# Optimization experiments

Hardware: AMD Instinct MI355X
Metric: run time of the kernel (lower is better)

The kernel has to match this reference:

```python
import jax, jax.numpy as jnp
import numpy as np

D_MODEL = 1024
N_HEADS = 16
D_K = D_MODEL // N_HEADS
THETA = 10000.0
BATCH = 2
SEQ = 2048


def apply_rope(x, positions):
    # x: [B, H, S, d_k], positions: [S] int
    half = D_K // 2
    inv_freq = 1.0 / (THETA ** (jnp.arange(half, dtype=jnp.float32) * 2.0 / D_K))  # [half]
    ang = positions.astype(jnp.float32)[:, None] * inv_freq[None, :]  # [S, half]
    cos = jnp.cos(ang)
    sin = jnp.sin(ang)
    xr = x.reshape(x.shape[:-1] + (half, 2))
    x1, x2 = xr[..., 0], xr[..., 1]
    o1 = x1 * cos - x2 * sin
    o2 = x1 * sin + x2 * cos
    return jnp.stack([o1, o2], axis=-1).reshape(x.shape)


def setup_inputs() -> dict:
    key = jax.random.key(0)
    ks = jax.random.split(key, 5)
    scale = 1.0 / np.sqrt(D_MODEL)
    return {
        "x": jax.random.normal(ks[0], (BATCH, SEQ, D_MODEL), jnp.float32),
        "token_positions": jnp.arange(SEQ, dtype=jnp.int32),
        "Wq": jax.random.normal(ks[1], (D_MODEL, D_MODEL), jnp.float32) * scale,
        "Wk": jax.random.normal(ks[2], (D_MODEL, D_MODEL), jnp.float32) * scale,
        "Wv": jax.random.normal(ks[3], (D_MODEL, D_MODEL), jnp.float32) * scale,
        "Wo": jax.random.normal(ks[4], (D_MODEL, D_MODEL), jnp.float32) * scale,
    }


def reference(x, token_positions, Wq, Wk, Wv, Wo):
    B, S, _ = x.shape
    # projections (Linear with weight [out, in], no bias): y = x @ W^T
    def split_heads(t):
        return t.reshape(B, S, N_HEADS, D_K).transpose(0, 2, 1, 3)  # [B,H,S,d_k]

    Q = split_heads(x @ Wq.T)
    K = split_heads(x @ Wk.T)
    V = split_heads(x @ Wv.T)

    Q = apply_rope(Q, token_positions)
    K = apply_rope(K, token_positions)

    scores = jnp.einsum("bhqd,bhkd->bhqk", Q, K) / np.sqrt(D_K)
    causal = jnp.tril(jnp.ones((S, S), dtype=bool))
    scores = jnp.where(causal, scores, -jnp.inf)
    attn = jax.nn.softmax(scores, axis=-1)
    out = jnp.einsum("bhqk,bhkd->bhqd", attn, V)  # [B,H,S,d_k]
    out = out.transpose(0, 2, 1, 3).reshape(B, S, D_MODEL)
    return out @ Wo.T
```

## Files before the change

kernel.cpp:

```cpp
#include <hip/hip_runtime.h>
#include <hip/hip_bf16.h>


typedef __bf16 bf16x8 __attribute__((ext_vector_type(8)));
typedef __bf16 bf16x4 __attribute__((ext_vector_type(4)));
typedef float f32x4 __attribute__((ext_vector_type(4)));
typedef unsigned short ushort8 __attribute__((ext_vector_type(8)));

#define BATCH 2
#define SEQ 2048
#define NH 16
#define DK 64
#define DM 1024
#define BH (BATCH*NH)
#define M_TOT (BATCH*SEQ)
#define QB 128

__device__ __forceinline__ void gload16(const void* g, void* l) {
    __builtin_amdgcn_global_load_lds((const __attribute__((address_space(1))) void*)g,
                                     (__attribute__((address_space(3))) void*)l, 16, 0, 0);
}

__global__ void cvt_kernel(const float* __restrict__ s, __bf16* __restrict__ d, int n) {
    int i = (blockIdx.x * blockDim.x + threadIdx.x) * 4;
    if (i >= n) return;
    float4 v = *(const float4*)(s + i);
    bf16x4 o;
    o[0] = (__bf16)v.x; o[1] = (__bf16)v.y; o[2] = (__bf16)v.z; o[3] = (__bf16)v.w;
    *(bf16x4*)(d + i) = o;
}

__global__ void cvt4_kernel(const float* __restrict__ s0, const float* __restrict__ s1,
                            const float* __restrict__ s2, const float* __restrict__ s3,
                            __bf16* __restrict__ d0, __bf16* __restrict__ d1,
                            __bf16* __restrict__ d2, __bf16* __restrict__ d3, int n) {
    const int z = blockIdx.y;
    const float* s = (z == 0) ? s0 : (z == 1) ? s1 : (z == 2) ? s2 : s3;
    __bf16* d = (z == 0) ? d0 : (z == 1) ? d1 : (z == 2) ? d2 : d3;
    int i = (blockIdx.x * blockDim.x + threadIdx.x) * 4;
    if (i >= n) return;
    float4 v = *(const float4*)(s + i);
    bf16x4 o;
    o[0] = (__bf16)v.x; o[1] = (__bf16)v.y; o[2] = (__bf16)v.z; o[3] = (__bf16)v.w;
    *(bf16x4*)(d + i) = o;
}

__device__ __forceinline__ void gemm_tile_compute(
    const __bf16* __restrict__ A, const __bf16* __restrict__ W,
    int m0, int n0, int K, __bf16* sA, __bf16* sB, f32x4 (&acc)[4][4])
{
    const int t = threadIdx.x;
    const int lane = t & 63, wid = t >> 6;
    const int wr = wid >> 1, wc = wid & 1;
    const int g = lane >> 4, l15 = lane & 15;

    f32x4 zero = {0.f, 0.f, 0.f, 0.f};
#pragma unroll
    for (int mt = 0; mt < 4; ++mt)
#pragma unroll
        for (int nt = 0; nt < 4; ++nt) acc[mt][nt] = zero;

    for (int k0 = 0; k0 < K; k0 += 32) {
        __syncthreads();
#pragma unroll
        for (int rnd = 0; rnd < 2; ++rnd) {
            int s = rnd * 256 + t;
            int row = s >> 2, ch = s & 3;
            __bf16* dstA = sA + (rnd * 256 + wid * 64) * 8;
            __bf16* dstB = sB + (rnd * 256 + wid * 64) * 8;
            gload16(A + (size_t)(m0 + row) * K + k0 + ch * 8, dstA);
            gload16(W + (size_t)(n0 + row) * K + k0 + ch * 8, dstB);
        }
        __syncthreads();
        bf16x8 af[4], bfr[4];
#pragma unroll
        for (int mt = 0; mt < 4; ++mt)
            af[mt] = *(const bf16x8*)&sA[(wr * 64 + mt * 16 + l15) * 32 + g * 8];
#pragma unroll
        for (int nt = 0; nt < 4; ++nt)
            bfr[nt] = *(const bf16x8*)&sB[(wc * 64 + nt * 16 + l15) * 32 + g * 8];
#pragma unroll
        for (int mt = 0; mt < 4; ++mt)
#pragma unroll
            for (int nt = 0; nt < 4; ++nt)
                acc[mt][nt] = __builtin_amdgcn_mfma_f32_16x16x32_bf16(af[mt], bfr[nt], acc[mt][nt], 0, 0, 0);
    }
}

__global__ __launch_bounds__(256) void gemm_qkv(
    const __bf16* __restrict__ xb,
    const __bf16* __restrict__ wq, const __bf16* __restrict__ wk, const __bf16* __restrict__ wv,
    __bf16* __restrict__ Qb, __bf16* __restrict__ Kb, __bf16* __restrict__ VTb)
{
    __shared__ __align__(16) __bf16 sA[128 * 32], sB[128 * 32];
    const int z = blockIdx.z;
    const __bf16* W = (z == 0) ? wq : ((z == 1) ? wk : wv);
    f32x4 acc[4][4];
    const int m0 = blockIdx.y * 128, n0 = blockIdx.x * 128;
    gemm_tile_compute(xb, W, m0, n0, DM, sA, sB, acc);

    const int t = threadIdx.x, lane = t & 63, wid = t >> 6;
    const int wr = wid >> 1, wc = wid & 1, g = lane >> 4, l15 = lane & 15;
    __bf16* QK = (z == 0) ? Qb : Kb;
#pragma unroll
    for (int mt = 0; mt < 4; ++mt)
#pragma unroll
        for (int nt = 0; nt < 4; ++nt)
#pragma unroll
            for (int r = 0; r < 4; ++r) {
                int m = m0 + wr * 64 + mt * 16 + g * 4 + r;
                int n = n0 + wc * 64 + nt * 16 + l15;
                int b = m >> 11, s = m & 2047, h = n >> 6, d = n & 63;
                __bf16 v = (__bf16)acc[mt][nt][r];
                if (z < 2)
                    QK[(((size_t)(b * NH + h)) * SEQ + s) * DK + d] = v;
                else
                    VTb[(((size_t)(b * NH + h)) * DK + d) * SEQ + s] = v;
            }
}

__global__ __launch_bounds__(256) void gemm_out(
    const __bf16* __restrict__ AO, const __bf16* __restrict__ wo, float* __restrict__ out)
{
    __shared__ __align__(16) __bf16 sA[128 * 32], sB[128 * 32];
    f32x4 acc[4][4];
    const int m0 = blockIdx.y * 128, n0 = blockIdx.x * 128;
    gemm_tile_compute(AO, wo, m0, n0, DM, sA, sB, acc);

    const int t = threadIdx.x, lane = t & 63, wid = t >> 6;
    const int wr = wid >> 1, wc = wid & 1, g = lane >> 4, l15 = lane & 15;
#pragma unroll
    for (int mt = 0; mt < 4; ++mt)
#pragma unroll
        for (int nt = 0; nt < 4; ++nt)
#pragma unroll
            for (int r = 0; r < 4; ++r) {
                int m = m0 + wr * 64 + mt * 16 + g * 4 + r;
                int n = n0 + wc * 64 + nt * 16 + l15;
                out[(size_t)m * DM + n] = acc[mt][nt][r];
            }
}

__global__ __launch_bounds__(256) void rope_kernel(
    __bf16* __restrict__ Qb, __bf16* __restrict__ Kb, const int* __restrict__ pos)
{
    __shared__ float ctab[32], stab[32];
    const int s = blockIdx.x;
    const int t = threadIdx.x;
    if (t < 32) {
        float invf = exp2f(-13.287712379549449f * (float)t * (1.0f / 32.0f));
        float ang = (float)pos[s] * invf;
        float sn, cs;
        sincosf(ang, &sn, &cs);
        ctab[t] = cs; stab[t] = sn;
    }
    __syncthreads();
#pragma unroll
    for (int u = 0; u < 8; ++u) {
        int id = u * 256 + t;
        int i = id & 31;
        int bh = (id >> 5) & 31;
        __bf16* P = (id >> 10) ? Kb : Qb;
        __bf16* p = P + ((size_t)bh * SEQ + s) * DK + i * 2;
        float x1 = (float)p[0], x2 = (float)p[1];
        float c = ctab[i], sn = stab[i];
        p[0] = (__bf16)(x1 * c - x2 * sn);
        p[1] = (__bf16)(x1 * sn + x2 * c);
    }
}

__global__ __launch_bounds__(256, 3) void attn_kernel(
    const __bf16* __restrict__ Qb, const __bf16* __restrict__ Kb,
    const __bf16* __restrict__ VTb, __bf16* __restrict__ AO)
{
    __shared__ __align__(16) __bf16 sK[2][64 * 64];
    __shared__ __align__(16) __bf16 sV[2][64 * 64];
    __shared__ __align__(16) __bf16 sP[4 * 2 * 16 * 64];

    const int n = blockIdx.x + 16 * blockIdx.y;
    const int xcd = n & 7, slot = n >> 3;
    const int bh = xcd * 4 + (slot >> 4);
    const int j = 15 - (slot & 15);
    const int t = threadIdx.x, lane = t & 63, wid = t >> 6;
    const int g = lane >> 4, l15 = lane & 15;

    const size_t baseQK = (size_t)bh * SEQ * DK;
    const size_t baseVT = (size_t)bh * DK * SEQ;
    const int b = bh >> 4, h = bh & 15;
    const int qrow_w = j * QB + wid * 32;

    bf16x8 qf[2][2];
#pragma unroll
    for (int s = 0; s < 2; ++s) {
        const __bf16* qp = Qb + baseQK + (size_t)(qrow_w + s * 16 + l15) * DK;
        qf[s][0] = *(const bf16x8*)(qp + g * 8);
        qf[s][1] = *(const bf16x8*)(qp + 32 + g * 8);
    }

    f32x4 zero = {0.f, 0.f, 0.f, 0.f};
    f32x4 oacc[2][4];
    float mrow[2][4], lrow[2][4];
#pragma unroll
    for (int s = 0; s < 2; ++s)
#pragma unroll
        for (int r = 0; r < 4; ++r) {
            oacc[s][r] = zero;
        }
#pragma unroll
    for (int s = 0; s < 2; ++s)
#pragma unroll
        for (int dt = 0; dt < 4; ++dt) oacc[s][dt] = zero;
#pragma unroll
    for (int s = 0; s < 2; ++s)
#pragma unroll
        for (int r = 0; r < 4; ++r) { mrow[s][r] = -3e38f; lrow[s][r] = 0.f; }

    const char* Kt0 = (const char*)(Kb + baseQK);
    const char* Vt0 = (const char*)(VTb + baseVT);
    const int ktmax = 2 * j + 1;

    auto stage_tile = [&](int kt, int bq) {
        const char* Kt = Kt0 + (size_t)kt * 64 * 128;
        const char* Vt = Vt0 + (size_t)kt * 128;
#pragma unroll
        for (int cc = 0; cc < 2; ++cc) {
            int c = t + cc * 256;
            int r = c >> 3, pp = c & 7;
            int p = pp ^ (r & 7);
            char* bK = (char*)sK[bq] + (cc * 256 + wid * 64) * 16;
            char* bV = (char*)sV[bq] + (cc * 256 + wid * 64) * 16;
            gload16(Kt + (size_t)r * 128 + p * 16, bK);
            gload16(Vt + (size_t)r * (SEQ * 2) + p * 16, bV);
        }
    };

    stage_tile(0, 0);
    __syncthreads();
    int cur = 0;

    for (int kt = 0; kt <= ktmax; ++kt) {
        if (kt < ktmax) stage_tile(kt + 1, cur ^ 1);

        f32x4 sacc[2][4];
#pragma unroll
        for (int s = 0; s < 2; ++s)
#pragma unroll
            for (int nt = 0; nt < 4; ++nt) sacc[s][nt] = zero;
#pragma unroll
        for (int nt = 0; nt < 4; ++nt) {
            int row = nt * 16 + l15;
#pragma unroll
            for (int ks = 0; ks < 2; ++ks) {
                bf16x8 kf = *(const bf16x8*)((const char*)sK[cur] + row * 128 +
                                             ((ks * 64 + g * 16) ^ ((row & 7) << 4)));
                sacc[0][nt] = __builtin_amdgcn_mfma_f32_16x16x32_bf16(qf[0][ks], kf, sacc[0][nt], 0, 0, 0);
                sacc[1][nt] = __builtin_amdgcn_mfma_f32_16x16x32_bf16(qf[1][ks], kf, sacc[1][nt], 0, 0, 0);
            }
        }

#pragma unroll
        for (int s = 0; s < 2; ++s) {
            const int q0 = qrow_w + s * 16;
            if (kt * 64 + 63 > q0) {
#pragma unroll
                for (int nt = 0; nt < 4; ++nt)
#pragma unroll
                    for (int r = 0; r < 4; ++r) {
                        int kv = kt * 64 + nt * 16 + l15;
                        int q = q0 + g * 4 + r;
                        if (kv > q) sacc[s][nt][r] = -3e38f; else sacc[s][nt][r] *= 0.125f;
                    }
            } else {
#pragma unroll
                for (int nt = 0; nt < 4; ++nt)
#pragma unroll
                    for (int r = 0; r < 4; ++r) sacc[s][nt][r] *= 0.125f;
            }
#pragma unroll
            for (int r = 0; r < 4; ++r) {
                float tm = fmaxf(fmaxf(sacc[s][0][r], sacc[s][1][r]),
                                 fmaxf(sacc[s][2][r], sacc[s][3][r]));
#pragma unroll
                for (int msk = 1; msk < 16; msk <<= 1) tm = fmaxf(tm, __shfl_xor(tm, msk));
                float mnew = fmaxf(mrow[s][r], tm);
                float sc = __expf(mrow[s][r] - mnew);
                float rs = 0.f;
#pragma unroll
                for (int nt = 0; nt < 4; ++nt) {
                    float p = __expf(sacc[s][nt][r] - mnew);
                    sacc[s][nt][r] = p;
                    rs += p;
                }
#pragma unroll
                for (int msk = 1; msk < 16; msk <<= 1) rs += __shfl_xor(rs, msk);
                lrow[s][r] = lrow[s][r] * sc + rs;
                mrow[s][r] = mnew;
#pragma unroll
                for (int dt = 0; dt < 4; ++dt) oacc[s][dt][r] *= sc;
            }
            char* myP = (char*)sP + (wid * 2 + s) * 2048;
#pragma unroll
            for (int nt = 0; nt < 4; ++nt)
#pragma unroll
                for (int r = 0; r < 4; ++r) {
                    int row = g * 4 + r;
                    *(__bf16*)(myP + row * 128 +
                               ((nt * 32 + l15 * 2) ^ ((row & 7) << 4))) = (__bf16)sacc[s][nt][r];
                }
        }

#pragma unroll
        for (int ks = 0; ks < 2; ++ks) {
            bf16x8 pf[2];
#pragma unroll
            for (int s = 0; s < 2; ++s)
                pf[s] = *(const bf16x8*)((char*)sP + (wid * 2 + s) * 2048 + l15 * 128 +
                                         ((ks * 64 + g * 16) ^ ((l15 & 7) << 4)));
#pragma unroll
            for (int dt = 0; dt < 4; ++dt) {
                int row = dt * 16 + l15;
                bf16x8 vf = *(const bf16x8*)((const char*)sV[cur] + row * 128 +
                                             ((ks * 64 + g * 16) ^ ((row & 7) << 4)));
                oacc[0][dt] = __builtin_amdgcn_mfma_f32_16x16x32_bf16(pf[0], vf, oacc[0][dt], 0, 0, 0);
                oacc[1][dt] = __builtin_amdgcn_mfma_f32_16x16x32_bf16(pf[1], vf, oacc[1][dt], 0, 0, 0);
            }
        }

        __syncthreads();
        cur ^= 1;
    }

#pragma unroll
    for (int s = 0; s < 2; ++s)
#pragma unroll
        for (int r = 0; r < 4; ++r) {
            float inv = 1.0f / lrow[s][r];
            int srow = qrow_w + s * 16 + g * 4 + r;
            size_t obase = ((size_t)b * SEQ + srow) * DM + h * DK;
#pragma unroll
            for (int dt = 0; dt < 4; ++dt)
                AO[obase + dt * 16 + l15] = (__bf16)(oacc[s][dt][r] * inv);
        }
}

extern "C" void kernel_launch(void* const* d_in, const int* in_sizes, int n_in,
                              void* d_out, int out_size, void* d_ws, size_t ws_size,
                              hipStream_t stream) {
    (void)in_sizes; (void)n_in; (void)out_size; (void)ws_size;
    const float* x  = (const float*)d_in[0];
    const int*  pos = (const int*)d_in[1];
    const float* Wq = (const float*)d_in[2];
    const float* Wk = (const float*)d_in[3];
    const float* Wv = (const float*)d_in[4];
    const float* Wo = (const float*)d_in[5];
    float* out = (float*)d_out;

    char* ws = (char*)d_ws;
    __bf16* xb  = (__bf16*)ws; ws += (size_t)M_TOT * DM * 2;
    __bf16* wqb = (__bf16*)ws; ws += (size_t)DM * DM * 2;
    __bf16* wkb = (__bf16*)ws; ws += (size_t)DM * DM * 2;
    __bf16* wvb = (__bf16*)ws; ws += (size_t)DM * DM * 2;
    __bf16* wob = (__bf16*)ws; ws += (size_t)DM * DM * 2;
    __bf16* Qb  = (__bf16*)ws; ws += (size_t)BH * SEQ * DK * 2;
    __bf16* Kb  = (__bf16*)ws; ws += (size_t)BH * SEQ * DK * 2;
    __bf16* VTb = (__bf16*)ws; ws += (size_t)BH * SEQ * DK * 2;
    __bf16* AOb = (__bf16*)ws; ws += (size_t)M_TOT * DM * 2;

    const int nx = M_TOT * DM, nw = DM * DM;
    cvt_kernel<<<nx / 4 / 256, 256, 0, stream>>>(x, xb, nx);
    cvt4_kernel<<<dim3(nw / 4 / 256, 4), 256, 0, stream>>>(Wq, Wk, Wv, Wo, wqb, wkb, wvb, wob, nw);

    gemm_qkv<<<dim3(DM / 128, M_TOT / 128, 3), 256, 0, stream>>>(xb, wqb, wkb, wvb, Qb, Kb, VTb);
    rope_kernel<<<SEQ, 256, 0, stream>>>(Qb, Kb, pos);
    attn_kernel<<<dim3(16, BH), 256, 0, stream>>>(Qb, Kb, VTb, AOb);
    gemm_out<<<dim3(DM / 128, M_TOT / 128), 256, 0, stream>>>(AOb, wob, out);
}
```

Measured before the change: 269.3 us.

## Widen GEMM K-tile with swizzled LDS, fuse QKV weights, pair attention query blocks

The shared GEMM tile now stages 64-wide K chunks into XOR-swizzled LDS, which halves the number of barrier rounds and avoids bank conflicts. Q/K/V weights go into one contiguous buffer, so a single 2D grid with XCD-aware block remapping covers all three projections, and gemm_out gets the same remap. The attention kernel launches 256 blocks, each handling a short and a long causal query block (j and 15-j) to balance work per block, and the occupancy hint of 3 is dropped. The wider LDS tiles and the loss of the occupancy bound may reduce waves per CU.

```diff
diff --git a/kernel.cpp b/kernel.cpp
--- a/kernel.cpp
+++ b/kernel.cpp
@@ -60,48 +60,57 @@
 #pragma unroll
         for (int nt = 0; nt < 4; ++nt) acc[mt][nt] = zero;
 
-    for (int k0 = 0; k0 < K; k0 += 32) {
+    for (int k0 = 0; k0 < K; k0 += 64) {
         __syncthreads();
 #pragma unroll
-        for (int rnd = 0; rnd < 2; ++rnd) {
-            int s = rnd * 256 + t;
-            int row = s >> 2, ch = s & 3;
-            __bf16* dstA = sA + (rnd * 256 + wid * 64) * 8;
-            __bf16* dstB = sB + (rnd * 256 + wid * 64) * 8;
-            gload16(A + (size_t)(m0 + row) * K + k0 + ch * 8, dstA);
-            gload16(W + (size_t)(n0 + row) * K + k0 + ch * 8, dstB);
+        for (int rnd = 0; rnd < 4; ++rnd) {
+            int slot = rnd * 256 + t;
+            int row = slot >> 3, pp = slot & 7;
+            int p = pp ^ (row & 7);
+            char* dA = (char*)sA + (rnd * 256 + wid * 64) * 16;
+            char* dB = (char*)sB + (rnd * 256 + wid * 64) * 16;
+            gload16((const char*)(A + (size_t)(m0 + row) * K + k0) + p * 16, dA);
+            gload16((const char*)(W + (size_t)(n0 + row) * K + k0) + p * 16, dB);
         }
         __syncthreads();
-        bf16x8 af[4], bfr[4];
-#pragma unroll
-        for (int mt = 0; mt < 4; ++mt)
-            af[mt] = *(const bf16x8*)&sA[(wr * 64 + mt * 16 + l15) * 32 + g * 8];
-#pragma unroll
-        for (int nt = 0; nt < 4; ++nt)
-            bfr[nt] = *(const bf16x8*)&sB[(wc * 64 + nt * 16 + l15) * 32 + g * 8];
-#pragma unroll
-        for (int mt = 0; mt < 4; ++mt)
-#pragma unroll
-            for (int nt = 0; nt < 4; ++nt)
-                acc[mt][nt] = __builtin_amdgcn_mfma_f32_16x16x32_bf16(af[mt], bfr[nt], acc[mt][nt], 0, 0, 0);
+#pragma unroll
+        for (int ks = 0; ks < 2; ++ks) {
+            bf16x8 af[4], bfr[4];
+#pragma unroll
+            for (int mt = 0; mt < 4; ++mt) {
+                int row = wr * 64 + mt * 16 + l15;
+                af[mt] = *(const bf16x8*)((char*)sA + row * 128 +
+                                          ((ks * 64 + g * 16) ^ ((row & 7) << 4)));
+            }
+#pragma unroll
+            for (int nt = 0; nt < 4; ++nt) {
+                int row = wc * 64 + nt * 16 + l15;
+                bfr[nt] = *(const bf16x8*)((char*)sB + row * 128 +
+                                           ((ks * 64 + g * 16) ^ ((row & 7) << 4)));
+            }
+#pragma unroll
+            for (int mt = 0; mt < 4; ++mt)
+#pragma unroll
+                for (int nt = 0; nt < 4; ++nt)
+                    acc[mt][nt] = __builtin_amdgcn_mfma_f32_16x16x32_bf16(af[mt], bfr[nt], acc[mt][nt], 0, 0, 0);
+        }
     }
 }
 
 __global__ __launch_bounds__(256) void gemm_qkv(
-    const __bf16* __restrict__ xb,
-    const __bf16* __restrict__ wq, const __bf16* __restrict__ wk, const __bf16* __restrict__ wv,
+    const __bf16* __restrict__ xb, const __bf16* __restrict__ wqkv,
     __bf16* __restrict__ Qb, __bf16* __restrict__ Kb, __bf16* __restrict__ VTb)
 {
-    __shared__ __align__(16) __bf16 sA[128 * 32], sB[128 * 32];
-    const int z = blockIdx.z;
-    const __bf16* W = (z == 0) ? wq : ((z == 1) ? wk : wv);
+    __shared__ __align__(16) __bf16 sA[128 * 64], sB[128 * 64];
+    int id = blockIdx.x + 24 * blockIdx.y;
+    id = (id & 7) * 96 + (id >> 3);
+    const int m0 = (id / 24) * 128, n0 = (id % 24) * 128;
+
     f32x4 acc[4][4];
-    const int m0 = blockIdx.y * 128, n0 = blockIdx.x * 128;
-    gemm_tile_compute(xb, W, m0, n0, DM, sA, sB, acc);
+    gemm_tile_compute(xb, wqkv, m0, n0, DM, sA, sB, acc);
 
     const int t = threadIdx.x, lane = t & 63, wid = t >> 6;
     const int wr = wid >> 1, wc = wid & 1, g = lane >> 4, l15 = lane & 15;
-    __bf16* QK = (z == 0) ? Qb : Kb;
 #pragma unroll
     for (int mt = 0; mt < 4; ++mt)
 #pragma unroll
@@ -110,10 +119,13 @@
             for (int r = 0; r < 4; ++r) {
                 int m = m0 + wr * 64 + mt * 16 + g * 4 + r;
                 int n = n0 + wc * 64 + nt * 16 + l15;
-                int b = m >> 11, s = m & 2047, h = n >> 6, d = n & 63;
+                int z = n >> 10, hd = n & 1023, h = hd >> 6, d = hd & 63;
+                int b = m >> 11, s = m & 2047;
                 __bf16 v = (__bf16)acc[mt][nt][r];
-                if (z < 2)
-                    QK[(((size_t)(b * NH + h)) * SEQ + s) * DK + d] = v;
+                if (z == 0)
+                    Qb[(((size_t)(b * NH + h)) * SEQ + s) * DK + d] = v;
+                else if (z == 1)
+                    Kb[(((size_t)(b * NH + h)) * SEQ + s) * DK + d] = v;
                 else
                     VTb[(((size_t)(b * NH + h)) * DK + d) * SEQ + s] = v;
             }
@@ -122,9 +134,12 @@
 __global__ __launch_bounds__(256) void gemm_out(
     const __bf16* __restrict__ AO, const __bf16* __restrict__ wo, float* __restrict__ out)
 {
-    __shared__ __align__(16) __bf16 sA[128 * 32], sB[128 * 32];
+    __shared__ __align__(16) __bf16 sA[128 * 64], sB[128 * 64];
+    int id = blockIdx.x + 8 * blockIdx.y;
+    id = (id & 7) * 32 + (id >> 3);
+    const int m0 = (id / 8) * 128, n0 = (id % 8) * 128;
+
     f32x4 acc[4][4];
-    const int m0 = blockIdx.y * 128, n0 = blockIdx.x * 128;
     gemm_tile_compute(AO, wo, m0, n0, DM, sA, sB, acc);
 
     const int t = threadIdx.x, lane = t & 63, wid = t >> 6;
@@ -169,7 +184,7 @@
     }
 }
 
-__global__ __launch_bounds__(256, 3) void attn_kernel(
+__global__ __launch_bounds__(256) void attn_kernel(
     const __bf16* __restrict__ Qb, const __bf16* __restrict__ Kb,
     const __bf16* __restrict__ VTb, __bf16* __restrict__ AO)
 {
@@ -177,47 +192,20 @@
     __shared__ __align__(16) __bf16 sV[2][64 * 64];
     __shared__ __align__(16) __bf16 sP[4 * 2 * 16 * 64];
 
-    const int n = blockIdx.x + 16 * blockIdx.y;
+    const int n = blockIdx.x;
     const int xcd = n & 7, slot = n >> 3;
-    const int bh = xcd * 4 + (slot >> 4);
-    const int j = 15 - (slot & 15);
+    const int bh = xcd * 4 + (slot >> 3);
+    const int x = slot & 7;
     const int t = threadIdx.x, lane = t & 63, wid = t >> 6;
     const int g = lane >> 4, l15 = lane & 15;
 
     const size_t baseQK = (size_t)bh * SEQ * DK;
     const size_t baseVT = (size_t)bh * DK * SEQ;
     const int b = bh >> 4, h = bh & 15;
-    const int qrow_w = j * QB + wid * 32;
-
-    bf16x8 qf[2][2];
-#pragma unroll
-    for (int s = 0; s < 2; ++s) {
-        const __bf16* qp = Qb + baseQK + (size_t)(qrow_w + s * 16 + l15) * DK;
-        qf[s][0] = *(const bf16x8*)(qp + g * 8);
-        qf[s][1] = *(const bf16x8*)(qp + 32 + g * 8);
-    }
-
-    f32x4 zero = {0.f, 0.f, 0.f, 0.f};
-    f32x4 oacc[2][4];
-    float mrow[2][4], lrow[2][4];
-#pragma unroll
-    for (int s = 0; s < 2; ++s)
-#pragma unroll
-        for (int r = 0; r < 4; ++r) {
-            oacc[s][r] = zero;
-        }
-#pragma unroll
-    for (int s = 0; s < 2; ++s)
-#pragma unroll
-        for (int dt = 0; dt < 4; ++dt) oacc[s][dt] = zero;
-#pragma unroll
-    for (int s = 0; s < 2; ++s)
-#pragma unroll
-        for (int r = 0; r < 4; ++r) { mrow[s][r] = -3e38f; lrow[s][r] = 0.f; }
 
     const char* Kt0 = (const char*)(Kb + baseQK);
     const char* Vt0 = (const char*)(VTb + baseVT);
-    const int ktmax = 2 * j + 1;
+    f32x4 zero = {0.f, 0.f, 0.f, 0.f};
 
     auto stage_tile = [&](int kt, int bq) {
         const char* Kt = Kt0 + (size_t)kt * 64 * 128;
@@ -234,113 +222,138 @@
         }
     };
 
-    stage_tile(0, 0);
-    __syncthreads();
-    int cur = 0;
-
-    for (int kt = 0; kt <= ktmax; ++kt) {
-        if (kt < ktmax) stage_tile(kt + 1, cur ^ 1);
-
-        f32x4 sacc[2][4];
+    for (int ph = 0; ph < 2; ++ph) {
+        const int j = ph ? (15 - x) : x;
+        const int qrow_w = j * QB + wid * 32;
+        const int ktmax = 2 * j + 1;
+
+        bf16x8 qf[2][2];
+#pragma unroll
+        for (int s = 0; s < 2; ++s) {
+            const __bf16* qp = Qb + baseQK + (size_t)(qrow_w + s * 16 + l15) * DK;
+            qf[s][0] = *(const bf16x8*)(qp + g * 8);
+            qf[s][1] = *(const bf16x8*)(qp + 32 + g * 8);
+        }
+
+        f32x4 oacc[2][4];
+        float mrow[2][4], lrow[2][4];
 #pragma unroll
         for (int s = 0; s < 2; ++s)
 #pragma unroll
-            for (int nt = 0; nt < 4; ++nt) sacc[s][nt] = zero;
-#pragma unroll
-        for (int nt = 0; nt < 4; ++nt) {
-            int row = nt * 16 + l15;
+            for (int dt = 0; dt < 4; ++dt) oacc[s][dt] = zero;
+#pragma unroll
+        for (int s = 0; s < 2; ++s)
+#pragma unroll
+            for (int r = 0; r < 4; ++r) { mrow[s][r] = -3e38f; lrow[s][r] = 0.f; }
+
+        stage_tile(0, 0);
+        __syncthreads();
+        int cur = 0;
+
+        for (int kt = 0; kt <= ktmax; ++kt) {
+            if (kt < ktmax) stage_tile(kt + 1, cur ^ 1);
+
+            f32x4 sacc[2][4];
+#pragma unroll
+            for (int s = 0; s < 2; ++s)
+#pragma unroll
+                for (int nt = 0; nt < 4; ++nt) sacc[s][nt] = zero;
+#pragma unroll
+            for (int nt = 0; nt < 4; ++nt) {
+                int row = nt * 16 + l15;
+#pragma unroll
+                for (int ks = 0; ks < 2; ++ks) {
+                    bf16x8 kf = *(const bf16x8*)((const char*)sK[cur] + row * 128 +
+                                                 ((ks * 64 + g * 16) ^ ((row & 7) << 4)));
+                    sacc[0][nt] = __builtin_amdgcn_mfma_f32_16x16x32_bf16(qf[0][ks], kf, sacc[0][nt], 0, 0, 0);
+                    sacc[1][nt] = __builtin_amdgcn_mfma_f32_16x16x32_bf16(qf[1][ks], kf, sacc[1][nt], 0, 0, 0);
+                }
+            }
+
+#pragma unroll
+            for (int s = 0; s < 2; ++s) {
+                const int q0 = qrow_w + s * 16;
+                if (kt * 64 + 63 > q0) {
+#pragma unroll
+                    for (int nt = 0; nt < 4; ++nt)
+#pragma unroll
+                        for (int r = 0; r < 4; ++r) {
+                            int kv = kt * 64 + nt * 16 + l15;
+                            int q = q0 + g * 4 + r;
+                            if (kv > q) sacc[s][nt][r] = -3e38f; else sacc[s][nt][r] *= 0.125f;
+                        }
+                } else {
+#pragma unroll
+                    for (int nt = 0; nt < 4; ++nt)
+#pragma unroll
+                        for (int r = 0; r < 4; ++r) sacc[s][nt][r] *= 0.125f;
+                }
+#pragma unroll
+                for (int r = 0; r < 4; ++r) {
+                    float tm = fmaxf(fmaxf(sacc[s][0][r], sacc[s][1][r]),
+                                     fmaxf(sacc[s][2][r], sacc[s][3][r]));
+#pragma unroll
+                    for (int msk = 1; msk < 16; msk <<= 1) tm = fmaxf(tm, __shfl_xor(tm, msk));
+                    float mnew = fmaxf(mrow[s][r], tm);
+                    float sc = __expf(mrow[s][r] - mnew);
+                    float rs = 0.f;
+#pragma unroll
+                    for (int nt = 0; nt < 4; ++nt) {
+                        float p = __expf(sacc[s][nt][r] - mnew);
+                        sacc[s][nt][r] = p;
+                        rs += p;
+                    }
+#pragma unroll
+                    for (int msk = 1; msk < 16; msk <<= 1) rs += __shfl_xor(rs, msk);
+                    lrow[s][r] = lrow[s][r] * sc + rs;
+                    mrow[s][r] = mnew;
+#pragma unroll
+                    for (int dt = 0; dt < 4; ++dt) oacc[s][dt][r] *= sc;
+                }
+                char* myP = (char*)sP + (wid * 2 + s) * 2048;
+#pragma unroll
+                for (int nt = 0; nt < 4; ++nt)
+#pragma unroll
+                    for (int r = 0; r < 4; ++r) {
+                        int row = g * 4 + r;
+                        *(__bf16*)(myP + row * 128 +
+                                   ((nt * 32 + l15 * 2) ^ ((row & 7) << 4))) = (__bf16)sacc[s][nt][r];
+                    }
+            }
+
 #pragma unroll
             for (int ks = 0; ks < 2; ++ks) {
-                bf16x8 kf = *(const bf16x8*)((const char*)sK[cur] + row * 128 +
-                                             ((ks * 64 + g * 16) ^ ((row & 7) << 4)));
-                sacc[0][nt] = __builtin_amdgcn_mfma_f32_16x16x32_bf16(qf[0][ks], kf, sacc[0][nt], 0, 0, 0);
-                sacc[1][nt] = __builtin_amdgcn_mfma_f32_16x16x32_bf16(qf[1][ks], kf, sacc[1][nt], 0, 0, 0);
-            }
-        }
-
-#pragma unroll
-        for (int s = 0; s < 2; ++s) {
-            const int q0 = qrow_w + s * 16;
-            if (kt * 64 + 63 > q0) {
-#pragma unroll
-                for (int nt = 0; nt < 4; ++nt)
-#pragma unroll
-                    for (int r = 0; r < 4; ++r) {
-                        int kv = kt * 64 + nt * 16 + l15;
-                        int q = q0 + g * 4 + r;
-                        if (kv > q) sacc[s][nt][r] = -3e38f; else sacc[s][nt][r] *= 0.125f;
-                    }
-            } else {
-#pragma unroll
-                for (int nt = 0; nt < 4; ++nt)
-#pragma unroll
-                    for (int r = 0; r < 4; ++r) sacc[s][nt][r] *= 0.125f;
-            }
+                bf16x8 pf[2];
+#pragma unroll
+                for (int s = 0; s < 2; ++s)
+                    pf[s] = *(const bf16x8*)((char*)sP + (wid * 2 + s) * 2048 + l15 * 128 +
+                                             ((ks * 64 + g * 16) ^ ((l15 & 7) << 4)));
+#pragma unroll
+                for (int dt = 0; dt < 4; ++dt) {
+                    int row = dt * 16 + l15;
+                    bf16x8 vf = *(const bf16x8*)((const char*)sV[cur] + row * 128 +
+                                                 ((ks * 64 + g * 16) ^ ((row & 7) << 4)));
+                    oacc[0][dt] = __builtin_amdgcn_mfma_f32_16x16x32_bf16(pf[0], vf, oacc[0][dt], 0, 0, 0);
+                    oacc[1][dt] = __builtin_amdgcn_mfma_f32_16x16x32_bf16(pf[1], vf, oacc[1][dt], 0, 0, 0);
+                }
+            }
+
+            __syncthreads();
+            cur ^= 1;
+        }
+
+#pragma unroll
+        for (int s = 0; s < 2; ++s)
 #pragma unroll
             for (int r = 0; r < 4; ++r) {
-                float tm = fmaxf(fmaxf(sacc[s][0][r], sacc[s][1][r]),
-                                 fmaxf(sacc[s][2][r], sacc[s][3][r]));
-#pragma unroll
-                for (int msk = 1; msk < 16; msk <<= 1) tm = fmaxf(tm, __shfl_xor(tm, msk));
-                float mnew = fmaxf(mrow[s][r], tm);
-                float sc = __expf(mrow[s][r] - mnew);
-                float rs = 0.f;
-#pragma unroll
-                for (int nt = 0; nt < 4; ++nt) {
-                    float p = __expf(sacc[s][nt][r] - mnew);
-                    sacc[s][nt][r] = p;
-                    rs += p;
-                }
-#pragma unroll
-                for (int msk = 1; msk < 16; msk <<= 1) rs += __shfl_xor(rs, msk);
-                lrow[s][r] = lrow[s][r] * sc + rs;
-                mrow[s][r] = mnew;
-#pragma unroll
-                for (int dt = 0; dt < 4; ++dt) oacc[s][dt][r] *= sc;
-            }
-            char* myP = (char*)sP + (wid * 2 + s) * 2048;
-#pragma unroll
-            for (int nt = 0; nt < 4; ++nt)
-#pragma unroll
-                for (int r = 0; r < 4; ++r) {
-                    int row = g * 4 + r;
-                    *(__bf16*)(myP + row * 128 +
-                               ((nt * 32 + l15 * 2) ^ ((row & 7) << 4))) = (__bf16)sacc[s][nt][r];
-                }
-        }
-
-#pragma unroll
-        for (int ks = 0; ks < 2; ++ks) {
-            bf16x8 pf[2];
-#pragma unroll
-            for (int s = 0; s < 2; ++s)
-                pf[s] = *(const bf16x8*)((char*)sP + (wid * 2 + s) * 2048 + l15 * 128 +
-                                         ((ks * 64 + g * 16) ^ ((l15 & 7) << 4)));
-#pragma unroll
-            for (int dt = 0; dt < 4; ++dt) {
-                int row = dt * 16 + l15;
-                bf16x8 vf = *(const bf16x8*)((const char*)sV[cur] + row * 128 +
-                                             ((ks * 64 + g * 16) ^ ((row & 7) << 4)));
-                oacc[0][dt] = __builtin_amdgcn_mfma_f32_16x16x32_bf16(pf[0], vf, oacc[0][dt], 0, 0, 0);
-                oacc[1][dt] = __builtin_amdgcn_mfma_f32_16x16x32_bf16(pf[1], vf, oacc[1][dt], 0, 0, 0);
-            }
-        }
-
-        __syncthreads();
-        cur ^= 1;
+                float inv = 1.0f / lrow[s][r];
+                int srow = qrow_w + s * 16 + g * 4 + r;
+                size_t obase = ((size_t)b * SEQ + srow) * DM + h * DK;
+#pragma unroll
+                for (int dt = 0; dt < 4; ++dt)
+                    AO[obase + dt * 16 + l15] = (__bf16)(oacc[s][dt][r] * inv);
+            }
     }
-
-#pragma unroll
-    for (int s = 0; s < 2; ++s)
-#pragma unroll
-        for (int r = 0; r < 4; ++r) {
-            float inv = 1.0f / lrow[s][r];
-            int srow = qrow_w + s * 16 + g * 4 + r;
-            size_t obase = ((size_t)b * SEQ + srow) * DM + h * DK;
-#pragma unroll
-            for (int dt = 0; dt < 4; ++dt)
-                AO[obase + dt * 16 + l15] = (__bf16)(oacc[s][dt][r] * inv);
-        }
 }
 
 extern "C" void kernel_launch(void* const* d_in, const int* in_sizes, int n_in,
@@ -356,22 +369,21 @@
     float* out = (float*)d_out;
 
     char* ws = (char*)d_ws;
-    __bf16* xb  = (__bf16*)ws; ws += (size_t)M_TOT * DM * 2;
-    __bf16* wqb = (__bf16*)ws; ws += (size_t)DM * DM * 2;
-    __bf16* wkb = (__bf16*)ws; ws += (size_t)DM * DM * 2;
-    __bf16* wvb = (__bf16*)ws; ws += (size_t)DM * DM * 2;
-    __bf16* wob = (__bf16*)ws; ws += (size_t)DM * DM * 2;
-    __bf16* Qb  = (__bf16*)ws; ws += (size_t)BH * SEQ * DK * 2;
-    __bf16* Kb  = (__bf16*)ws; ws += (size_t)BH * SEQ * DK * 2;
-    __bf16* VTb = (__bf16*)ws; ws += (size_t)BH * SEQ * DK * 2;
-    __bf16* AOb = (__bf16*)ws; ws += (size_t)M_TOT * DM * 2;
+    __bf16* xb   = (__bf16*)ws; ws += (size_t)M_TOT * DM * 2;
+    __bf16* wqkv = (__bf16*)ws; ws += (size_t)3 * DM * DM * 2;
+    __bf16* wob  = (__bf16*)ws; ws += (size_t)DM * DM * 2;
+    __bf16* Qb   = (__bf16*)ws; ws += (size_t)BH * SEQ * DK * 2;
+    __bf16* Kb   = (__bf16*)ws; ws += (size_t)BH * SEQ * DK * 2;
+    __bf16* VTb  = (__bf16*)ws; ws += (size_t)BH * SEQ * DK * 2;
+    __bf16* AOb  = (__bf16*)ws; ws += (size_t)M_TOT * DM * 2;
 
     const int nx = M_TOT * DM, nw = DM * DM;
     cvt_kernel<<<nx / 4 / 256, 256, 0, stream>>>(x, xb, nx);
-    cvt4_kernel<<<dim3(nw / 4 / 256, 4), 256, 0, stream>>>(Wq, Wk, Wv, Wo, wqb, wkb, wvb, wob, nw);
-
-    gemm_qkv<<<dim3(DM / 128, M_TOT / 128, 3), 256, 0, stream>>>(xb, wqb, wkb, wvb, Qb, Kb, VTb);
+    cvt4_kernel<<<dim3(nw / 4 / 256, 4), 256, 0, stream>>>(
+        Wq, Wk, Wv, Wo, wqkv, wqkv + nw, wqkv + 2 * nw, wob, nw);
+
+    gemm_qkv<<<dim3(24, M_TOT / 128), 256, 0, stream>>>(xb, wqkv, Qb, Kb, VTb);
     rope_kernel<<<SEQ, 256, 0, stream>>>(Qb, Kb, pos);
-    attn_kernel<<<dim3(16, BH), 256, 0, stream>>>(Qb, Kb, VTb, AOb);
-    gemm_out<<<dim3(DM / 128, M_TOT / 128), 256, 0, stream>>>(AOb, wob, out);
-}
+    attn_kernel<<<256, 256, 0, stream>>>(Qb, Kb, VTb, AOb);
+    gemm_out<<<dim3(8, M_TOT / 128), 256, 0, stream>>>(AOb, wob, out);
+}
```

Result: faster. 263.0 us (-2.3%).
